# Kernel tuning notes

Hardware: AMD Instinct MI355X
Metric: run time of the kernel (lower is better)

## Reference

```python
import jax, jax.numpy as jnp
import numpy as np

N = 50000      # num_nodes
E = 800000     # num_edges (avg degree 16)
D = 128        # input_dim = hidden_dim = output_dim
L = 3          # num_layers
EPS = 1e-5     # BatchNorm eps


def setup_inputs() -> dict:
    key = jax.random.key(0)
    k_x, k_e, k_w, k_b = jax.random.split(key, 4)
    x = jax.random.normal(k_x, (N, D), dtype=jnp.float32)
    edge_index = jax.random.randint(k_e, (2, E), 0, N, dtype=jnp.int32)
    # Stacked per-layer params: GCN weight/bias + BatchNorm gamma/beta
    Ws = jax.random.normal(k_w, (L, D, D), dtype=jnp.float32) * (1.0 / np.sqrt(D))
    bs = jax.random.normal(k_b, (L, D), dtype=jnp.float32) * 0.01
    gammas = jnp.ones((L, D), dtype=jnp.float32)
    betas = jnp.zeros((L, D), dtype=jnp.float32)
    return {"x": x, "edge_index": edge_index, "Ws": Ws, "bs": bs,
            "gammas": gammas, "betas": betas}


def reference(x, edge_index, Ws, bs, gammas, betas):
    """CausalGNN forward: L x (GCNConv -> BN(train stats) -> ReLU[not last]) with residuals.
    Dropout p=0 (deterministic). GCNConv is PyG-style: add self-loops, symmetric
    D^{-1/2} (A+I) D^{-1/2} normalization, linear transform + bias."""
    src, dst = edge_index[0], edge_index[1]
    # degree including self-loop (+1), computed at aggregation index
    deg = jax.ops.segment_sum(jnp.ones((E,), jnp.float32), dst, num_segments=N) + 1.0
    dis = jax.lax.rsqrt(deg)                       # deg >= 1, safe
    norm = dis[src] * dis[dst]                      # [E] edge norm
    self_norm = dis * dis                           # [N] self-loop norm = 1/deg

    for i in range(L):
        h = x @ Ws[i]                               # [N, D]
        # scatter-add aggregation of normalized neighbor messages
        agg = jax.ops.segment_sum(h[src] * norm[:, None], dst, num_segments=N)
        agg = agg + self_norm[:, None] * h + bs[i]
        # BatchNorm1d (training mode: biased batch statistics over nodes)
        mean = jnp.mean(agg, axis=0)
        var = jnp.mean(jnp.square(agg - mean), axis=0)
        y = gammas[i] * (agg - mean) * jax.lax.rsqrt(var + EPS) + betas[i]
        if i < L - 1:
            y = jax.nn.relu(y)
        x = x + y if i > 0 else y                   # residual (dims match)
    return x
```

## Files before the change

kernel.cpp:

```cpp
#include <hip/hip_runtime.h>
#include <hip/hip_bf16.h>
#include <hip/hip_fp16.h>

#define N_ 50000
#define E_ 800000
#define D_ 128
#define L_ 3

#define GG 782
#define CB 3125

typedef _Float16 half8 __attribute__((ext_vector_type(8)));
typedef float f32x4 __attribute__((ext_vector_type(4)));


__device__ inline float4 hcvt(uint2 u) {
    __half2 h0 = *(__half2*)&u.x;
    __half2 h1 = *(__half2*)&u.y;
    float2 f0 = __half22float2(h0);
    float2 f1 = __half22float2(h1);
    return make_float4(f0.x, f0.y, f1.x, f1.y);
}

__device__ inline unsigned pkh(float a, float b) {
    __half2 h = __floats2half2_rn(a, b);
    return *(unsigned*)&h;
}

__device__ inline unsigned short pkh1(float a) {
    _Float16 h = (_Float16)a;
    return *(unsigned short*)&h;
}


__global__ void k_countw(const int* __restrict__ dst, int* __restrict__ deg,
                         int* __restrict__ offbuf,
                         const float* __restrict__ Ws, unsigned short* __restrict__ Wb) {
    int b = blockIdx.x;
    if (b < CB) {
        int e = b * 256 + threadIdx.x;
        offbuf[e] = atomicAdd(&deg[dst[e]], 1);
    } else {
        int l = b - CB;
        const float* Wl = Ws + l * 16384;
        unsigned short* Wo = Wb + l * 16384;
        for (int i = threadIdx.x; i < 16384; i += 256) {
            int n = i >> 7, k = i & 127;
            Wo[n * 128 + k] = pkh1(Wl[k * 128 + n]);
        }
    }
}


__global__ __launch_bounds__(1024) void k_scan1(const int* __restrict__ deg,
                                                int* __restrict__ linc,
                                                int* __restrict__ bsum,
                                                float* __restrict__ dis) {
    __shared__ int wsum[16];
    int t    = threadIdx.x;
    int lane = t & 63;
    int wid  = t >> 6;
    int i    = blockIdx.x * 1024 + t;
    int d    = (i < N_) ? deg[i] : 0;
    if (i < N_) dis[i] = rsqrtf((float)d + 1.0f);
    int v = d;
#pragma unroll
    for (int off = 1; off < 64; off <<= 1) {
        int u = __shfl_up(v, off);
        if (lane >= off) v += u;
    }
    if (lane == 63) wsum[wid] = v;
    __syncthreads();
    if (wid == 0) {
        int w = (lane < 16) ? wsum[lane] : 0;
#pragma unroll
        for (int off = 1; off < 16; off <<= 1) {
            int u = __shfl_up(w, off);
            if (lane >= off) w += u;
        }
        if (lane < 16) wsum[lane] = w;
    }
    __syncthreads();
    int woff = (wid > 0) ? wsum[wid - 1] : 0;
    v += woff;
    if (i < N_) linc[i] = v;
    if (t == 1023) bsum[blockIdx.x] = v;
}

__global__ __launch_bounds__(1024) void k_scan3(const int* __restrict__ linc,
                                                const int* __restrict__ bsum,
                                                int* __restrict__ row_ptr) {
    __shared__ int sboff;
    int t = threadIdx.x;
    if (t < 64) {
        int v = (t < 49) ? bsum[t] : 0;
#pragma unroll
        for (int off = 1; off < 64; off <<= 1) {
            int u = __shfl_up(v, off);
            if (t >= off) v += u;
        }
        int ex = (blockIdx.x == 0) ? 0 : __shfl(v, (int)blockIdx.x - 1, 64);
        if (t == 0) sboff = ex;
    }
    __syncthreads();
    int i = blockIdx.x * 1024 + t;
    if (i < N_) row_ptr[i + 1] = linc[i] + sboff;
    if (i == 0) row_ptr[0] = 0;
}


__device__ __forceinline__ void gemm_body(const float* __restrict__ Xin,
                                          const unsigned short* __restrict__ XinH,
                                          const unsigned short* __restrict__ Wb,
                                          const float* __restrict__ dis,
                                          uint4* __restrict__ Hb,
                                          const float* __restrict__ st,
                                          const float* __restrict__ gamma,
                                          const float* __restrict__ beta,
                                          const unsigned short* __restrict__ resH,
                                          unsigned short* __restrict__ xoutH,
                                          int blk) {
    __shared__ unsigned short wt[128 * 136];
    __shared__ unsigned short xb[64 * 136];
    __shared__ float sab[256];
    int t  = threadIdx.x;
    int r0 = blk * 64;

    if (st) {
        if (t < 128) {
            float s = 0.f, s2 = 0.f;
#pragma unroll
            for (int k = 0; k < 8; ++k) {
                s  += st[k * 256 + t];
                s2 += st[k * 256 + 128 + t];
            }
            float mean = s * (1.0f / N_);
            float var  = s2 * (1.0f / N_) - mean * mean;
            float a = gamma[t] * rsqrtf(var + 1e-5f);
            sab[t]       = a;
            sab[128 + t] = beta[t] - mean * a;
        }
        __syncthreads();
    }

#pragma unroll
    for (int j = 0; j < 8; ++j) {
        int i = t + 256 * j;
        int row = i >> 4, c16 = i & 15;
        *(uint4*)&wt[row * 136 + c16 * 8] = ((const uint4*)Wb)[i];
    }
#pragma unroll
    for (int j = 0; j < 8; ++j) {
        int g   = t + 256 * j;
        int row = g >> 5;
        int c4  = (g & 31) * 4;
        int gr  = r0 + row;
        float4 v = make_float4(0.f, 0.f, 0.f, 0.f);
        if (gr < N_) {
            if (XinH) v = hcvt(*(const uint2*)(XinH + gr * 128 + c4));
            else      v = *(const float4*)(Xin + gr * 128 + c4);
            if (st) {
                v.x = fmaxf(sab[c4] * v.x + sab[128 + c4], 0.f);
                v.y = fmaxf(sab[c4 + 1] * v.y + sab[128 + c4 + 1], 0.f);
                v.z = fmaxf(sab[c4 + 2] * v.z + sab[128 + c4 + 2], 0.f);
                v.w = fmaxf(sab[c4 + 3] * v.w + sab[128 + c4 + 3], 0.f);
                if (resH) {
                    float4 rr = hcvt(*(const uint2*)(resH + gr * 128 + c4));
                    v.x += rr.x; v.y += rr.y; v.z += rr.z; v.w += rr.w;
                }
            }
        }
        uint2 p;
        p.x = pkh(v.x, v.y);
        p.y = pkh(v.z, v.w);
        if (st && gr < N_) *(uint2*)(xoutH + gr * 128 + c4) = p;
        *(uint2*)&xb[row * 136 + c4] = p;
    }
    __syncthreads();

    int wv   = t >> 6;
    int lane = t & 63;
    int ln   = lane & 15;
    int quad = lane >> 4;

    const unsigned short* arow = &xb[(wv * 16 + ln) * 136 + quad * 8];
    half8 af[4];
#pragma unroll
    for (int ks = 0; ks < 4; ++ks) af[ks] = *(const half8*)(arow + ks * 32);

    f32x4 acc[8];
#pragma unroll
    for (int ct = 0; ct < 8; ++ct) acc[ct] = (f32x4){0.f, 0.f, 0.f, 0.f};

#pragma unroll
    for (int ct = 0; ct < 8; ++ct) {
        const unsigned short* wp = &wt[(ct * 16 + ln) * 136 + quad * 8];
#pragma unroll
        for (int ks = 0; ks < 4; ++ks) {
            half8 bf = *(const half8*)(wp + ks * 32);
            acc[ct] = __builtin_amdgcn_mfma_f32_16x16x32_f16(af[ks], bf, acc[ct], 0, 0, 0);
        }
    }

    float dr[4];
#pragma unroll
    for (int reg = 0; reg < 4; ++reg) {
        int r = r0 + wv * 16 + quad * 4 + reg;
        dr[reg] = dis[r < N_ ? r : (N_ - 1)];
    }
    __syncthreads();
#pragma unroll
    for (int ct = 0; ct < 8; ++ct) {
#pragma unroll
        for (int reg = 0; reg < 4; ++reg) {
            int lrow = wv * 16 + quad * 4 + reg;
            xb[lrow * 136 + ct * 16 + ln] = pkh1(acc[ct][reg] * dr[reg]);
        }
    }
    __syncthreads();
#pragma unroll
    for (int j = 0; j < 4; ++j) {
        int i = t + 256 * j;
        int row = i >> 4, c16 = i & 15;
        int gr = r0 + row;
        if (gr < N_) Hb[gr * 16 + c16] = *(uint4*)&xb[row * 136 + c16 * 8];
    }
}


__global__ __launch_bounds__(256) void k_fillg(const int* __restrict__ src,
                                               const int* __restrict__ dst,
                                               const int* __restrict__ row_ptr,
                                               const int* __restrict__ offbuf,
                                               int* __restrict__ csr_src,
                                               const float* __restrict__ x,
                                               const unsigned short* __restrict__ Wb,
                                               const float* __restrict__ dis,
                                               uint4* __restrict__ Hb) {
    int b = blockIdx.x;
    if (b < GG) {
        gemm_body(x, nullptr, Wb, dis, Hb, nullptr, nullptr, nullptr, nullptr, nullptr, b);
    } else {
        int e = (b - GG) * 256 + threadIdx.x;
        int d = dst[e];
        csr_src[row_ptr[d] + offbuf[e]] = src[e];
    }
}


__global__ __launch_bounds__(256) void k_gemm(const unsigned short* __restrict__ XinH,
                                              const unsigned short* __restrict__ Wb,
                                              const float* __restrict__ dis,
                                              uint4* __restrict__ Hb,
                                              const float* __restrict__ st,
                                              const float* __restrict__ gamma,
                                              const float* __restrict__ beta,
                                              const unsigned short* __restrict__ resH,
                                              unsigned short* __restrict__ xoutH) {
    gemm_body(nullptr, XinH, Wb, dis, Hb, st, gamma, beta, resH, xoutH, blockIdx.x);
}


__global__ __launch_bounds__(256) void k_agg(const uint4* __restrict__ Hb,
                                             const int* __restrict__ row_ptr,
                                             const int* __restrict__ csr_src,
                                             const float* __restrict__ dis,
                                             const float* __restrict__ bias,
                                             uint4* __restrict__ AGGh,
                                             float* __restrict__ stats2) {
    int tid  = threadIdx.x;
    int sub  = tid >> 4;
    int lane = tid & 15;
    int node = blockIdx.x * 16 + sub;

    int beg = row_ptr[node], end = row_ptr[node + 1];
    uint4 su = Hb[node * 16 + lane];
    float4 acc0 = hcvt(make_uint2(su.x, su.y));
    float4 acc1 = hcvt(make_uint2(su.z, su.w));

    for (int c = beg; c < end; c += 16) {
        int m = end - c; if (m > 16) m = 16;
        int idx = (lane < m) ? csr_src[c + lane] : 0;
        int j = 0;
        for (; j + 8 <= m; j += 8) {
            int s0 = __shfl(idx, j, 16);
            int s1 = __shfl(idx, j + 1, 16);
            int s2 = __shfl(idx, j + 2, 16);
            int s3 = __shfl(idx, j + 3, 16);
            int s4 = __shfl(idx, j + 4, 16);
            int s5 = __shfl(idx, j + 5, 16);
            int s6 = __shfl(idx, j + 6, 16);
            int s7 = __shfl(idx, j + 7, 16);
            uint4 a0 = Hb[s0 * 16 + lane];
            uint4 a1 = Hb[s1 * 16 + lane];
            uint4 a2 = Hb[s2 * 16 + lane];
            uint4 a3 = Hb[s3 * 16 + lane];
            uint4 a4 = Hb[s4 * 16 + lane];
            uint4 a5 = Hb[s5 * 16 + lane];
            uint4 a6 = Hb[s6 * 16 + lane];
            uint4 a7 = Hb[s7 * 16 + lane];
            float4 f00 = hcvt(make_uint2(a0.x, a0.y)), f01 = hcvt(make_uint2(a0.z, a0.w));
            float4 f10 = hcvt(make_uint2(a1.x, a1.y)), f11 = hcvt(make_uint2(a1.z, a1.w));
            float4 f20 = hcvt(make_uint2(a2.x, a2.y)), f21 = hcvt(make_uint2(a2.z, a2.w));
            float4 f30 = hcvt(make_uint2(a3.x, a3.y)), f31 = hcvt(make_uint2(a3.z, a3.w));
            float4 f40 = hcvt(make_uint2(a4.x, a4.y)), f41 = hcvt(make_uint2(a4.z, a4.w));
            float4 f50 = hcvt(make_uint2(a5.x, a5.y)), f51 = hcvt(make_uint2(a5.z, a5.w));
            float4 f60 = hcvt(make_uint2(a6.x, a6.y)), f61 = hcvt(make_uint2(a6.z, a6.w));
            float4 f70 = hcvt(make_uint2(a7.x, a7.y)), f71 = hcvt(make_uint2(a7.z, a7.w));
            acc0.x += (f00.x + f10.x) + (f20.x + f30.x) + (f40.x + f50.x) + (f60.x + f70.x);
            acc0.y += (f00.y + f10.y) + (f20.y + f30.y) + (f40.y + f50.y) + (f60.y + f70.y);
            acc0.z += (f00.z + f10.z) + (f20.z + f30.z) + (f40.z + f50.z) + (f60.z + f70.z);
            acc0.w += (f00.w + f10.w) + (f20.w + f30.w) + (f40.w + f50.w) + (f60.w + f70.w);
            acc1.x += (f01.x + f11.x) + (f21.x + f31.x) + (f41.x + f51.x) + (f61.x + f71.x);
            acc1.y += (f01.y + f11.y) + (f21.y + f31.y) + (f41.y + f51.y) + (f61.y + f71.y);
            acc1.z += (f01.z + f11.z) + (f21.z + f31.z) + (f41.z + f51.z) + (f61.z + f71.z);
            acc1.w += (f01.w + f11.w) + (f21.w + f31.w) + (f41.w + f51.w) + (f61.w + f71.w);
        }
        for (; j + 4 <= m; j += 4) {
            int s0 = __shfl(idx, j, 16);
            int s1 = __shfl(idx, j + 1, 16);
            int s2 = __shfl(idx, j + 2, 16);
            int s3 = __shfl(idx, j + 3, 16);
            uint4 a0 = Hb[s0 * 16 + lane];
            uint4 a1 = Hb[s1 * 16 + lane];
            uint4 a2 = Hb[s2 * 16 + lane];
            uint4 a3 = Hb[s3 * 16 + lane];
            float4 f00 = hcvt(make_uint2(a0.x, a0.y)), f01 = hcvt(make_uint2(a0.z, a0.w));
            float4 f10 = hcvt(make_uint2(a1.x, a1.y)), f11 = hcvt(make_uint2(a1.z, a1.w));
            float4 f20 = hcvt(make_uint2(a2.x, a2.y)), f21 = hcvt(make_uint2(a2.z, a2.w));
            float4 f30 = hcvt(make_uint2(a3.x, a3.y)), f31 = hcvt(make_uint2(a3.z, a3.w));
            acc0.x += f00.x + f10.x + f20.x + f30.x;
            acc0.y += f00.y + f10.y + f20.y + f30.y;
            acc0.z += f00.z + f10.z + f20.z + f30.z;
            acc0.w += f00.w + f10.w + f20.w + f30.w;
            acc1.x += f01.x + f11.x + f21.x + f31.x;
            acc1.y += f01.y + f11.y + f21.y + f31.y;
            acc1.z += f01.z + f11.z + f21.z + f31.z;
            acc1.w += f01.w + f11.w + f21.w + f31.w;
        }
        for (; j < m; ++j) {
            int s0 = __shfl(idx, j, 16);
            uint4 a0 = Hb[s0 * 16 + lane];
            float4 f00 = hcvt(make_uint2(a0.x, a0.y)), f01 = hcvt(make_uint2(a0.z, a0.w));
            acc0.x += f00.x; acc0.y += f00.y; acc0.z += f00.z; acc0.w += f00.w;
            acc1.x += f01.x; acc1.y += f01.y; acc1.z += f01.z; acc1.w += f01.w;
        }
    }

    float dn = dis[node];
    float4 b0 = *(const float4*)(bias + lane * 8);
    float4 b1 = *(const float4*)(bias + lane * 8 + 4);
    float4 r0, r1;
    r0.x = dn * acc0.x + b0.x; r0.y = dn * acc0.y + b0.y;
    r0.z = dn * acc0.z + b0.z; r0.w = dn * acc0.w + b0.w;
    r1.x = dn * acc1.x + b1.x; r1.y = dn * acc1.y + b1.y;
    r1.z = dn * acc1.z + b1.z; r1.w = dn * acc1.w + b1.w;
    uint4 o;
    o.x = pkh(r0.x, r0.y); o.y = pkh(r0.z, r0.w);
    o.z = pkh(r1.x, r1.y); o.w = pkh(r1.z, r1.w);
    AGGh[node * 16 + lane] = o;

    __shared__ float sbuf[16][128];
    float4* sp = (float4*)&sbuf[sub][lane * 8];
    sp[0] = r0; sp[1] = r1;
    __syncthreads();
    if (tid < 128) {
        float s = 0.f, s2 = 0.f;
#pragma unroll
        for (int k = 0; k < 16; ++k) {
            float v = sbuf[k][tid];
            s += v; s2 += v * v;
        }
        float* stp = stats2 + (blockIdx.x & 7) * 256;
        atomicAdd(&stp[tid], s);
        atomicAdd(&stp[128 + tid], s2);
    }
}


__global__ __launch_bounds__(256) void k_normF(const uint4* __restrict__ AGGh,
                                               const uint4* __restrict__ resH,
                                               const float* __restrict__ st,
                                               const float* __restrict__ gamma,
                                               const float* __restrict__ beta,
                                               float4* __restrict__ OUT) {
    __shared__ float sab[256];
    int t = threadIdx.x;
    if (t < 128) {
        float s = 0.f, s2 = 0.f;
#pragma unroll
        for (int k = 0; k < 8; ++k) {
            s  += st[k * 256 + t];
            s2 += st[k * 256 + 128 + t];
        }
        float mean = s * (1.0f / N_);
        float var  = s2 * (1.0f / N_) - mean * mean;
        float a = gamma[t] * rsqrtf(var + 1e-5f);
        sab[t]       = a;
        sab[128 + t] = beta[t] - mean * a;
    }
    __syncthreads();
    for (int i = blockIdx.x * 256 + t; i < N_ * 16; i += gridDim.x * 256) {
        int f8 = (i & 15) * 8;
        uint4 va = AGGh[i];
        uint4 vr = resH[i];
        float4 a0 = hcvt(make_uint2(va.x, va.y)), a1 = hcvt(make_uint2(va.z, va.w));
        float4 q0 = hcvt(make_uint2(vr.x, vr.y)), q1 = hcvt(make_uint2(vr.z, vr.w));
        float4 o0, o1;
        o0.x = sab[f8] * a0.x + sab[128 + f8] + q0.x;
        o0.y = sab[f8 + 1] * a0.y + sab[128 + f8 + 1] + q0.y;
        o0.z = sab[f8 + 2] * a0.z + sab[128 + f8 + 2] + q0.z;
        o0.w = sab[f8 + 3] * a0.w + sab[128 + f8 + 3] + q0.w;
        o1.x = sab[f8 + 4] * a1.x + sab[128 + f8 + 4] + q1.x;
        o1.y = sab[f8 + 5] * a1.y + sab[128 + f8 + 5] + q1.y;
        o1.z = sab[f8 + 6] * a1.z + sab[128 + f8 + 6] + q1.z;
        o1.w = sab[f8 + 7] * a1.w + sab[128 + f8 + 7] + q1.w;
        OUT[i * 2]     = o0;
        OUT[i * 2 + 1] = o1;
    }
}


extern "C" void kernel_launch(void* const* d_in, const int* in_sizes, int n_in,
                              void* d_out, int out_size, void* d_ws, size_t ws_size,
                              hipStream_t stream) {
    const float* x      = (const float*)d_in[0];
    const int*   ei     = (const int*)d_in[1];
    const float* Ws     = (const float*)d_in[2];
    const float* bs     = (const float*)d_in[3];
    const float* gammas = (const float*)d_in[4];
    const float* betas  = (const float*)d_in[5];
    float* out = (float*)d_out;

    const int* src = ei;
    const int* dst = ei + E_;

    char* w = (char*)d_ws;
    int*   deg     = (int*)(w + 0);
    float* stats2  = (float*)(w + 200000);
    int*   row_ptr = (int*)(w + 224576);
    float* dis     = (float*)(w + 424592);
    int*   offbuf  = (int*)(w + 624592);
    int*   csr_src = (int*)(w + 3824592);
    uint4* Hb      = (uint4*)(w + 7024640);
    unsigned short* XBh = (unsigned short*)(w + 19824640);
    unsigned short* Wb  = (unsigned short*)(w + 32624640);
    uint4* AGGh    = (uint4*)(w + 32723072);

    int* linc = (int*)XBh;
    int* bsum = (int*)XBh + N_;

    hipMemsetAsync(d_ws, 0, 224576, stream);

    k_countw<<<CB + 3, 256, 0, stream>>>(dst, deg, offbuf, Ws, Wb);
    k_scan1<<<49, 1024, 0, stream>>>(deg, linc, bsum, dis);
    k_scan3<<<49, 1024, 0, stream>>>(linc, bsum, row_ptr);
    k_fillg<<<GG + CB, 256, 0, stream>>>(src, dst, row_ptr, offbuf, csr_src,
                                         x, Wb, dis, Hb);

    k_agg<<<N_ / 16, 256, 0, stream>>>(Hb, row_ptr, csr_src, dis, bs,
                                       AGGh, stats2);
    k_gemm<<<GG, 256, 0, stream>>>((const unsigned short*)AGGh, Wb + 16384, dis, Hb,
                                   stats2, gammas, betas, nullptr, XBh);
    k_agg<<<N_ / 16, 256, 0, stream>>>(Hb, row_ptr, csr_src, dis, bs + D_,
                                       AGGh, stats2 + 2048);
    k_gemm<<<GG, 256, 0, stream>>>((const unsigned short*)AGGh, Wb + 32768, dis, Hb,
                                   stats2 + 2048, gammas + D_, betas + D_, XBh, XBh);
    k_agg<<<N_ / 16, 256, 0, stream>>>(Hb, row_ptr, csr_src, dis, bs + 2 * D_,
                                       AGGh, stats2 + 4096);
    k_normF<<<1024, 256, 0, stream>>>(AGGh, (const uint4*)XBh,
                                      stats2 + 4096, gammas + 2 * D_, betas + 2 * D_,
                                      (float4*)out);
}
```

Baseline: 295.9 us.

## Split H into feature-quarter planes and gather four edges per 16-lane group

The GEMM epilogue now writes H as four feature-sliced planes of 32 halfs (64 bytes) per node. The aggregation kernel loops over these planes, and each 16-lane group gathers four edges at once, each lane loading 16 bytes of one edge's slice, then reduces partial sums with shuffles. The aim is better cache locality per plane pass and more independent loads in flight. In exchange the CSR indices are reread four times, extra shuffle reductions are added, and each row gather becomes a 64-byte segment rather than 256 bytes.

```diff
diff --git a/kernel.cpp b/kernel.cpp
--- a/kernel.cpp
+++ b/kernel.cpp
@@ -220,10 +220,11 @@
     __syncthreads();
 #pragma unroll
     for (int j = 0; j < 4; ++j) {
-        int i = t + 256 * j;
-        int row = i >> 4, c16 = i & 15;
-        int gr = r0 + row;
-        if (gr < N_) Hb[gr * 16 + c16] = *(uint4*)&xb[row * 136 + c16 * 8];
+        int n_local = t >> 2;
+        int q = t & 3;
+        int gr = r0 + n_local;
+        if (gr < N_)
+            Hb[j * (N_ * 4) + gr * 4 + q] = *(uint4*)&xb[n_local * 136 + j * 32 + q * 8];
     }
 }
 
@@ -268,101 +269,98 @@
                                              const float* __restrict__ bias,
                                              uint4* __restrict__ AGGh,
                                              float* __restrict__ stats2) {
-    int tid  = threadIdx.x;
-    int sub  = tid >> 4;
-    int lane = tid & 15;
-    int node = blockIdx.x * 16 + sub;
+    int tid   = threadIdx.x;
+    int sub   = tid >> 4;
+    int lane  = tid & 15;
+    int eslot = lane >> 2;
+    int fgrp  = lane & 3;
+    int node  = blockIdx.x * 16 + sub;
 
     int beg = row_ptr[node], end = row_ptr[node + 1];
-    uint4 su = Hb[node * 16 + lane];
-    float4 acc0 = hcvt(make_uint2(su.x, su.y));
-    float4 acc1 = hcvt(make_uint2(su.z, su.w));
-
-    for (int c = beg; c < end; c += 16) {
-        int m = end - c; if (m > 16) m = 16;
-        int idx = (lane < m) ? csr_src[c + lane] : 0;
-        int j = 0;
-        for (; j + 8 <= m; j += 8) {
-            int s0 = __shfl(idx, j, 16);
-            int s1 = __shfl(idx, j + 1, 16);
-            int s2 = __shfl(idx, j + 2, 16);
-            int s3 = __shfl(idx, j + 3, 16);
-            int s4 = __shfl(idx, j + 4, 16);
-            int s5 = __shfl(idx, j + 5, 16);
-            int s6 = __shfl(idx, j + 6, 16);
-            int s7 = __shfl(idx, j + 7, 16);
-            uint4 a0 = Hb[s0 * 16 + lane];
-            uint4 a1 = Hb[s1 * 16 + lane];
-            uint4 a2 = Hb[s2 * 16 + lane];
-            uint4 a3 = Hb[s3 * 16 + lane];
-            uint4 a4 = Hb[s4 * 16 + lane];
-            uint4 a5 = Hb[s5 * 16 + lane];
-            uint4 a6 = Hb[s6 * 16 + lane];
-            uint4 a7 = Hb[s7 * 16 + lane];
-            float4 f00 = hcvt(make_uint2(a0.x, a0.y)), f01 = hcvt(make_uint2(a0.z, a0.w));
-            float4 f10 = hcvt(make_uint2(a1.x, a1.y)), f11 = hcvt(make_uint2(a1.z, a1.w));
-            float4 f20 = hcvt(make_uint2(a2.x, a2.y)), f21 = hcvt(make_uint2(a2.z, a2.w));
-            float4 f30 = hcvt(make_uint2(a3.x, a3.y)), f31 = hcvt(make_uint2(a3.z, a3.w));
-            float4 f40 = hcvt(make_uint2(a4.x, a4.y)), f41 = hcvt(make_uint2(a4.z, a4.w));
-            float4 f50 = hcvt(make_uint2(a5.x, a5.y)), f51 = hcvt(make_uint2(a5.z, a5.w));
-            float4 f60 = hcvt(make_uint2(a6.x, a6.y)), f61 = hcvt(make_uint2(a6.z, a6.w));
-            float4 f70 = hcvt(make_uint2(a7.x, a7.y)), f71 = hcvt(make_uint2(a7.z, a7.w));
-            acc0.x += (f00.x + f10.x) + (f20.x + f30.x) + (f40.x + f50.x) + (f60.x + f70.x);
-            acc0.y += (f00.y + f10.y) + (f20.y + f30.y) + (f40.y + f50.y) + (f60.y + f70.y);
-            acc0.z += (f00.z + f10.z) + (f20.z + f30.z) + (f40.z + f50.z) + (f60.z + f70.z);
-            acc0.w += (f00.w + f10.w) + (f20.w + f30.w) + (f40.w + f50.w) + (f60.w + f70.w);
-            acc1.x += (f01.x + f11.x) + (f21.x + f31.x) + (f41.x + f51.x) + (f61.x + f71.x);
-            acc1.y += (f01.y + f11.y) + (f21.y + f31.y) + (f41.y + f51.y) + (f61.y + f71.y);
-            acc1.z += (f01.z + f11.z) + (f21.z + f31.z) + (f41.z + f51.z) + (f61.z + f71.z);
-            acc1.w += (f01.w + f11.w) + (f21.w + f31.w) + (f41.w + f51.w) + (f61.w + f71.w);
-        }
-        for (; j + 4 <= m; j += 4) {
-            int s0 = __shfl(idx, j, 16);
-            int s1 = __shfl(idx, j + 1, 16);
-            int s2 = __shfl(idx, j + 2, 16);
-            int s3 = __shfl(idx, j + 3, 16);
-            uint4 a0 = Hb[s0 * 16 + lane];
-            uint4 a1 = Hb[s1 * 16 + lane];
-            uint4 a2 = Hb[s2 * 16 + lane];
-            uint4 a3 = Hb[s3 * 16 + lane];
-            float4 f00 = hcvt(make_uint2(a0.x, a0.y)), f01 = hcvt(make_uint2(a0.z, a0.w));
-            float4 f10 = hcvt(make_uint2(a1.x, a1.y)), f11 = hcvt(make_uint2(a1.z, a1.w));
-            float4 f20 = hcvt(make_uint2(a2.x, a2.y)), f21 = hcvt(make_uint2(a2.z, a2.w));
-            float4 f30 = hcvt(make_uint2(a3.x, a3.y)), f31 = hcvt(make_uint2(a3.z, a3.w));
-            acc0.x += f00.x + f10.x + f20.x + f30.x;
-            acc0.y += f00.y + f10.y + f20.y + f30.y;
-            acc0.z += f00.z + f10.z + f20.z + f30.z;
-            acc0.w += f00.w + f10.w + f20.w + f30.w;
-            acc1.x += f01.x + f11.x + f21.x + f31.x;
-            acc1.y += f01.y + f11.y + f21.y + f31.y;
-            acc1.z += f01.z + f11.z + f21.z + f31.z;
-            acc1.w += f01.w + f11.w + f21.w + f31.w;
-        }
-        for (; j < m; ++j) {
-            int s0 = __shfl(idx, j, 16);
-            uint4 a0 = Hb[s0 * 16 + lane];
-            float4 f00 = hcvt(make_uint2(a0.x, a0.y)), f01 = hcvt(make_uint2(a0.z, a0.w));
-            acc0.x += f00.x; acc0.y += f00.y; acc0.z += f00.z; acc0.w += f00.w;
-            acc1.x += f01.x; acc1.y += f01.y; acc1.z += f01.z; acc1.w += f01.w;
-        }
-    }
-
     float dn = dis[node];
-    float4 b0 = *(const float4*)(bias + lane * 8);
-    float4 b1 = *(const float4*)(bias + lane * 8 + 4);
-    float4 r0, r1;
-    r0.x = dn * acc0.x + b0.x; r0.y = dn * acc0.y + b0.y;
-    r0.z = dn * acc0.z + b0.z; r0.w = dn * acc0.w + b0.w;
-    r1.x = dn * acc1.x + b1.x; r1.y = dn * acc1.y + b1.y;
-    r1.z = dn * acc1.z + b1.z; r1.w = dn * acc1.w + b1.w;
-    uint4 o;
-    o.x = pkh(r0.x, r0.y); o.y = pkh(r0.z, r0.w);
-    o.z = pkh(r1.x, r1.y); o.w = pkh(r1.z, r1.w);
-    AGGh[node * 16 + lane] = o;
 
     __shared__ float sbuf[16][128];
-    float4* sp = (float4*)&sbuf[sub][lane * 8];
-    sp[0] = r0; sp[1] = r1;
+
+#pragma unroll
+    for (int p = 0; p < 4; ++p) {
+        const uint4* Hp = Hb + p * (N_ * 4);
+        float4 acc0 = make_float4(0.f, 0.f, 0.f, 0.f);
+        float4 acc1 = make_float4(0.f, 0.f, 0.f, 0.f);
+
+        for (int c = beg; c < end; c += 16) {
+            int m = end - c; if (m > 16) m = 16;
+            int idx = (lane < m) ? csr_src[c + lane] : 0;
+            if (m == 16) {
+                int s0 = __shfl(idx, eslot, 16);
+                int s1 = __shfl(idx, 4 + eslot, 16);
+                int s2 = __shfl(idx, 8 + eslot, 16);
+                int s3 = __shfl(idx, 12 + eslot, 16);
+                uint4 a0 = Hp[s0 * 4 + fgrp];
+                uint4 a1 = Hp[s1 * 4 + fgrp];
+                uint4 a2 = Hp[s2 * 4 + fgrp];
+                uint4 a3 = Hp[s3 * 4 + fgrp];
+                float4 f00 = hcvt(make_uint2(a0.x, a0.y)), f01 = hcvt(make_uint2(a0.z, a0.w));
+                float4 f10 = hcvt(make_uint2(a1.x, a1.y)), f11 = hcvt(make_uint2(a1.z, a1.w));
+                float4 f20 = hcvt(make_uint2(a2.x, a2.y)), f21 = hcvt(make_uint2(a2.z, a2.w));
+                float4 f30 = hcvt(make_uint2(a3.x, a3.y)), f31 = hcvt(make_uint2(a3.z, a3.w));
+                acc0.x += (f00.x + f10.x) + (f20.x + f30.x);
+                acc0.y += (f00.y + f10.y) + (f20.y + f30.y);
+                acc0.z += (f00.z + f10.z) + (f20.z + f30.z);
+                acc0.w += (f00.w + f10.w) + (f20.w + f30.w);
+                acc1.x += (f01.x + f11.x) + (f21.x + f31.x);
+                acc1.y += (f01.y + f11.y) + (f21.y + f31.y);
+                acc1.z += (f01.z + f11.z) + (f21.z + f31.z);
+                acc1.w += (f01.w + f11.w) + (f21.w + f31.w);
+            } else {
+                for (int j = 0; j < m; j += 4) {
+                    int slot = j + eslot;
+                    int srcl = (slot < m) ? slot : (m - 1);
+                    int s = __shfl(idx, srcl, 16);
+                    uint4 a = Hp[s * 4 + fgrp];
+                    if (slot < m) {
+                        float4 f0 = hcvt(make_uint2(a.x, a.y));
+                        float4 f1 = hcvt(make_uint2(a.z, a.w));
+                        acc0.x += f0.x; acc0.y += f0.y; acc0.z += f0.z; acc0.w += f0.w;
+                        acc1.x += f1.x; acc1.y += f1.y; acc1.z += f1.z; acc1.w += f1.w;
+                    }
+                }
+            }
+        }
+
+#pragma unroll
+        for (int off = 8; off >= 4; off >>= 1) {
+            acc0.x += __shfl_down(acc0.x, off, 16);
+            acc0.y += __shfl_down(acc0.y, off, 16);
+            acc0.z += __shfl_down(acc0.z, off, 16);
+            acc0.w += __shfl_down(acc0.w, off, 16);
+            acc1.x += __shfl_down(acc1.x, off, 16);
+            acc1.y += __shfl_down(acc1.y, off, 16);
+            acc1.z += __shfl_down(acc1.z, off, 16);
+            acc1.w += __shfl_down(acc1.w, off, 16);
+        }
+
+        if (eslot == 0) {
+            uint4 su = Hp[node * 4 + fgrp];
+            float4 s0 = hcvt(make_uint2(su.x, su.y));
+            float4 s1 = hcvt(make_uint2(su.z, su.w));
+            acc0.x += s0.x; acc0.y += s0.y; acc0.z += s0.z; acc0.w += s0.w;
+            acc1.x += s1.x; acc1.y += s1.y; acc1.z += s1.z; acc1.w += s1.w;
+            int f0i = p * 32 + fgrp * 8;
+            float4 b0 = *(const float4*)(bias + f0i);
+            float4 b1 = *(const float4*)(bias + f0i + 4);
+            float4 r0, r1;
+            r0.x = dn * acc0.x + b0.x; r0.y = dn * acc0.y + b0.y;
+            r0.z = dn * acc0.z + b0.z; r0.w = dn * acc0.w + b0.w;
+            r1.x = dn * acc1.x + b1.x; r1.y = dn * acc1.y + b1.y;
+            r1.z = dn * acc1.z + b1.z; r1.w = dn * acc1.w + b1.w;
+            uint4 o;
+            o.x = pkh(r0.x, r0.y); o.y = pkh(r0.z, r0.w);
+            o.z = pkh(r1.x, r1.y); o.w = pkh(r1.z, r1.w);
+            AGGh[node * 16 + p * 4 + fgrp] = o;
+            *(float4*)&sbuf[sub][f0i]     = r0;
+            *(float4*)&sbuf[sub][f0i + 4] = r1;
+        }
+    }
     __syncthreads();
     if (tid < 128) {
         float s = 0.f, s2 = 0.f;
```

Result: slower. 338.0 us (+14.2%).
